# Kernel optimization log

Hardware: AMD Instinct MI355X
Metric: run time of the kernel (lower is better)

## Reference

```python
import jax, jax.numpy as jnp
import numpy as np

H_DIM = 64
NUM_SEQS = 4096
LEN_PATTERN = [16, 24, 32, 40, 48, 56, 64, 40]  # cycles; mean 40, max 64


def _make_seq_start_end():
    lens = np.tile(np.array(LEN_PATTERN, dtype=np.int64), NUM_SEQS // len(LEN_PATTERN))
    ends = np.cumsum(lens)
    starts = np.concatenate([[0], ends[:-1]])
    return np.stack([starts, ends], axis=1)  # [S, 2], total N = 163840


def setup_inputs() -> dict:
    key = jax.random.key(0)
    sse = _make_seq_start_end()
    n_total = int(sse[-1, 1])
    h_states = jax.random.normal(key, (1, n_total, H_DIM), dtype=jnp.float32)
    return {"h_states": h_states, "seq_start_end": jnp.asarray(sse)}


def reference(h_states, seq_start_end):
    # seq_start_end is a constant ragged-segment descriptor; use host values
    sse = np.asarray(jax.device_get(seq_start_end))
    starts = sse[:, 0]
    lens = sse[:, 1] - sse[:, 0]
    L = int(lens.max())              # max pedestrians per scene
    H = h_states.reshape(-1, h_states.shape[-1])  # [N, D]
    N, D = H.shape

    pos = np.arange(L)[None, :]                   # [1, L]
    valid = pos < lens[:, None]                   # [S, L] bool
    idx = starts[:, None] + pos                   # [S, L]
    gather_idx = jnp.asarray(np.where(valid, idx, 0))
    valid_j = jnp.asarray(valid)

    Hp = H[gather_idx]                            # [S, L, D] padded segments
    scores = jnp.einsum('sld,smd->slm', Hp, Hp)   # [S, L, L]
    neg = jnp.asarray(-1e30, dtype=scores.dtype)
    scores = jnp.where(valid_j[:, None, :], scores, neg)  # mask padded keys
    attn = jax.nn.softmax(scores, axis=-1)        # softmax over dim=1 of original (keys)
    ctx = jnp.einsum('slm,smd->sld', attn, Hp)    # [S, L, D]

    # scatter padded rows back to flat [N, D]; invalid rows go to dummy slot N
    flat_idx = jnp.asarray(np.where(valid, idx, N).reshape(-1))
    out = jnp.zeros((N + 1, D), dtype=ctx.dtype).at[flat_idx].set(ctx.reshape(-1, D))
    return out[:N]
```

## Files before the change

### kernel.cpp

```cpp
#include <hip/hip_runtime.h>

#define D 64
#define STR 72

typedef __attribute__((ext_vector_type(8))) short bf16x8;
typedef __attribute__((ext_vector_type(4))) float f32x4;
typedef __attribute__((ext_vector_type(4))) unsigned int u32x4;

static __device__ __forceinline__ unsigned short f2bf(float f) {
  unsigned u = __builtin_bit_cast(unsigned, f);
  u += 0x7fffu + ((u >> 16) & 1u);
  return (unsigned short)(u >> 16);
}

__global__ __launch_bounds__(64, 4)
void seq_attn_kernel(const float* __restrict__ h,
                     const int* __restrict__ sse,
                     float* __restrict__ out) {
  __shared__ unsigned short Hs[64 * STR];

  const int s = blockIdx.x;
  const int lane = threadIdx.x;
  const int start = sse[2 * s];
  const int L = sse[2 * s + 1] - start;
  const int nt = (L + 15) >> 4;
  const int g = lane >> 4;
  const int c16 = lane & 15;

  {
    const float* src = h + (size_t)start * D;
    const int c4 = c16 * 4;
    float4 va[8], vb[8];
    #pragma unroll
    for (int it = 0; it < 8; ++it) {
      const int r = it * 4 + g;
      const int rc = (r < L) ? r : 0;
      va[it] = *(const float4*)(src + rc * D + c4);
    }
    const bool hi = (L > 32);
    #pragma unroll
    for (int it = 0; it < 8; ++it) {
      const int r = 32 + it * 4 + g;
      const int rc = (r < L) ? r : 0;
      vb[it] = hi ? *(const float4*)(src + rc * D + c4) : make_float4(0.f, 0.f, 0.f, 0.f);
    }
    #pragma unroll
    for (int it = 0; it < 8; ++it) {
      const int r = it * 4 + g;
      const bool ok = (r < L);
      ushort4 w;
      w.x = ok ? f2bf(va[it].x) : (unsigned short)0;
      w.y = ok ? f2bf(va[it].y) : (unsigned short)0;
      w.z = ok ? f2bf(va[it].z) : (unsigned short)0;
      w.w = ok ? f2bf(va[it].w) : (unsigned short)0;
      *(ushort4*)&Hs[r * STR + c4] = w;
    }
    #pragma unroll
    for (int it = 0; it < 8; ++it) {
      const int r = 32 + it * 4 + g;
      const bool ok = (r < L);
      ushort4 w;
      w.x = ok ? f2bf(vb[it].x) : (unsigned short)0;
      w.y = ok ? f2bf(vb[it].y) : (unsigned short)0;
      w.z = ok ? f2bf(vb[it].z) : (unsigned short)0;
      w.w = ok ? f2bf(vb[it].w) : (unsigned short)0;
      *(ushort4*)&Hs[r * STR + c4] = w;
    }
  }
  __syncthreads();

  bf16x8 hf[4][2];
  #pragma unroll
  for (int t = 0; t < 4; ++t)
    #pragma unroll
    for (int kb = 0; kb < 2; ++kb)
      hf[t][kb] = *(const bf16x8*)&Hs[(t * 16 + c16) * STR + kb * 32 + g * 8];

  bf16x8 vf[4][2];
  #pragma unroll
  for (int t = 0; t < 4; ++t)
    #pragma unroll
    for (int kb = 0; kb < 2; ++kb) {
      u32x4 w;
      #pragma unroll
      for (int dd = 0; dd < 4; ++dd) {
        const int k0 = kb * 32 + g * 8 + 2 * dd;
        const unsigned lo = Hs[k0 * STR + t * 16 + c16];
        const unsigned hi2 = Hs[(k0 + 1) * STR + t * 16 + c16];
        w[dd] = lo | (hi2 << 16);
      }
      vf[t][kb] = __builtin_bit_cast(bf16x8, w);
    }

  #pragma unroll
  for (int ti = 0; ti < 4; ++ti) {
    if (ti >= nt) continue;

    f32x4 acc[4];
    #pragma unroll
    for (int tj = 0; tj < 4; ++tj) {
      f32x4 z = {0.f, 0.f, 0.f, 0.f};
      acc[tj] = z;
    }
    #pragma unroll
    for (int tj = 0; tj < 4; ++tj)
      #pragma unroll
      for (int kb = 0; kb < 2; ++kb)
        acc[tj] = __builtin_amdgcn_mfma_f32_16x16x32_bf16(
            hf[ti][kb], hf[tj][kb], acc[tj], 0, 0, 0);

    float inv[4];
    #pragma unroll
    for (int r = 0; r < 4; ++r) {
      float mx = -1e30f;
      #pragma unroll
      for (int tj = 0; tj < 4; ++tj) {
        const float sv = (tj * 16 + c16 < L) ? acc[tj][r] : -1e30f;
        acc[tj][r] = sv;
        mx = fmaxf(mx, sv);
      }
      #pragma unroll
      for (int off = 1; off < 16; off <<= 1)
        mx = fmaxf(mx, __shfl_xor(mx, off, 64));
      float sum = 0.f;
      #pragma unroll
      for (int tj = 0; tj < 4; ++tj) {
        const float p = __expf(acc[tj][r] - mx);
        acc[tj][r] = p;
        sum += p;
      }
      #pragma unroll
      for (int off = 1; off < 16; off <<= 1)
        sum += __shfl_xor(sum, off, 64);
      inv[r] = 1.0f / sum;
    }

    #pragma unroll
    for (int tj = 0; tj < 4; ++tj)
      #pragma unroll
      for (int r = 0; r < 4; ++r)
        Hs[(ti * 16 + g * 4 + r) * STR + tj * 16 + c16] = f2bf(acc[tj][r]);

    __syncthreads();

    bf16x8 pf[2];
    #pragma unroll
    for (int kb = 0; kb < 2; ++kb)
      pf[kb] = *(const bf16x8*)&Hs[(ti * 16 + c16) * STR + kb * 32 + g * 8];

    f32x4 o[4];
    #pragma unroll
    for (int tjd = 0; tjd < 4; ++tjd) {
      f32x4 z = {0.f, 0.f, 0.f, 0.f};
      o[tjd] = z;
    }
    #pragma unroll
    for (int tjd = 0; tjd < 4; ++tjd)
      #pragma unroll
      for (int kb = 0; kb < 2; ++kb)
        o[tjd] = __builtin_amdgcn_mfma_f32_16x16x32_bf16(
            pf[kb], vf[tjd][kb], o[tjd], 0, 0, 0);

    #pragma unroll
    for (int r = 0; r < 4; ++r) {
      const int row = ti * 16 + g * 4 + r;
      if (row < L) {
        float* dst = out + (size_t)(start + row) * D;
        const float sc = inv[r];
        #pragma unroll
        for (int tjd = 0; tjd < 4; ++tjd)
          dst[tjd * 16 + c16] = o[tjd][r] * sc;
      }
    }
  }
}

extern "C" void kernel_launch(void* const* d_in, const int* in_sizes, int n_in,
                              void* d_out, int out_size, void* d_ws, size_t ws_size,
                              hipStream_t stream) {
  const float* h = (const float*)d_in[0];
  const int* sse = (const int*)d_in[1];
  float* out = (float*)d_out;
  const int nseq = in_sizes[1] / 2;
  seq_attn_kernel<<<nseq, 64, 0, stream>>>(h, sse, out);
}
```

Measured before the change: 27.77 us.

## Pack four independent sequences per block, one per wave, drop barriers

Launches 256-thread blocks where each wave handles its own sequence with a private LDS slice, cutting the block count by four. Block-wide __syncthreads are replaced by an LDS waitcnt, since each wave only touches its own shared memory. This reduces block launch overhead and barrier cost. It relies on in-order LDS execution within a wave and on the sequence count being divisible by four.

```diff
diff --git a/kernel.cpp b/kernel.cpp
--- a/kernel.cpp
+++ b/kernel.cpp
@@ -2,6 +2,7 @@
 
 #define D 64
 #define STR 72
+#define WAVES 4
 
 typedef __attribute__((ext_vector_type(8))) short bf16x8;
 typedef __attribute__((ext_vector_type(4))) float f32x4;
@@ -13,14 +14,20 @@
   return (unsigned short)(u >> 16);
 }
 
-__global__ __launch_bounds__(64, 4)
+#define LDSWAIT() asm volatile("s_waitcnt lgkmcnt(0)" ::: "memory")
+
+__global__ __launch_bounds__(256, 4)
 void seq_attn_kernel(const float* __restrict__ h,
                      const int* __restrict__ sse,
                      float* __restrict__ out) {
-  __shared__ unsigned short Hs[64 * STR];
+  __shared__ unsigned short HsAll[WAVES * 64 * STR];
 
-  const int s = blockIdx.x;
-  const int lane = threadIdx.x;
+  const int tid = threadIdx.x;
+  const int w = tid >> 6;
+  const int lane = tid & 63;
+  unsigned short* Hs = HsAll + w * (64 * STR);
+
+  const int s = blockIdx.x + gridDim.x * w;
   const int start = sse[2 * s];
   const int L = sse[2 * s + 1] - start;
   const int nt = (L + 15) >> 4;
@@ -48,26 +55,26 @@
     for (int it = 0; it < 8; ++it) {
       const int r = it * 4 + g;
       const bool ok = (r < L);
-      ushort4 w;
-      w.x = ok ? f2bf(va[it].x) : (unsigned short)0;
-      w.y = ok ? f2bf(va[it].y) : (unsigned short)0;
-      w.z = ok ? f2bf(va[it].z) : (unsigned short)0;
-      w.w = ok ? f2bf(va[it].w) : (unsigned short)0;
-      *(ushort4*)&Hs[r * STR + c4] = w;
+      ushort4 wv;
+      wv.x = ok ? f2bf(va[it].x) : (unsigned short)0;
+      wv.y = ok ? f2bf(va[it].y) : (unsigned short)0;
+      wv.z = ok ? f2bf(va[it].z) : (unsigned short)0;
+      wv.w = ok ? f2bf(va[it].w) : (unsigned short)0;
+      *(ushort4*)&Hs[r * STR + c4] = wv;
     }
     #pragma unroll
     for (int it = 0; it < 8; ++it) {
       const int r = 32 + it * 4 + g;
       const bool ok = (r < L);
-      ushort4 w;
-      w.x = ok ? f2bf(vb[it].x) : (unsigned short)0;
-      w.y = ok ? f2bf(vb[it].y) : (unsigned short)0;
-      w.z = ok ? f2bf(vb[it].z) : (unsigned short)0;
-      w.w = ok ? f2bf(vb[it].w) : (unsigned short)0;
-      *(ushort4*)&Hs[r * STR + c4] = w;
+      ushort4 wv;
+      wv.x = ok ? f2bf(vb[it].x) : (unsigned short)0;
+      wv.y = ok ? f2bf(vb[it].y) : (unsigned short)0;
+      wv.z = ok ? f2bf(vb[it].z) : (unsigned short)0;
+      wv.w = ok ? f2bf(vb[it].w) : (unsigned short)0;
+      *(ushort4*)&Hs[r * STR + c4] = wv;
     }
   }
-  __syncthreads();
+  LDSWAIT();
 
   bf16x8 hf[4][2];
   #pragma unroll
@@ -81,15 +88,15 @@
   for (int t = 0; t < 4; ++t)
     #pragma unroll
     for (int kb = 0; kb < 2; ++kb) {
-      u32x4 w;
+      u32x4 wv;
       #pragma unroll
       for (int dd = 0; dd < 4; ++dd) {
         const int k0 = kb * 32 + g * 8 + 2 * dd;
         const unsigned lo = Hs[k0 * STR + t * 16 + c16];
         const unsigned hi2 = Hs[(k0 + 1) * STR + t * 16 + c16];
-        w[dd] = lo | (hi2 << 16);
+        wv[dd] = lo | (hi2 << 16);
       }
-      vf[t][kb] = __builtin_bit_cast(bf16x8, w);
+      vf[t][kb] = __builtin_bit_cast(bf16x8, wv);
     }
 
   #pragma unroll
@@ -141,7 +148,7 @@
       for (int r = 0; r < 4; ++r)
         Hs[(ti * 16 + g * 4 + r) * STR + tj * 16 + c16] = f2bf(acc[tj][r]);
 
-    __syncthreads();
+    LDSWAIT();
 
     bf16x8 pf[2];
     #pragma unroll
@@ -182,5 +189,6 @@
   const int* sse = (const int*)d_in[1];
   float* out = (float*)d_out;
   const int nseq = in_sizes[1] / 2;
-  seq_attn_kernel<<<nseq, 64, 0, stream>>>(h, sse, out);
+  const int nblk = nseq / WAVES;
+  seq_attn_kernel<<<nblk, 64 * WAVES, 0, stream>>>(h, sse, out);
 }
```

Measured after the change: 27.93 us. About the same (+0.6%).
